# Performance work log

Measured on AMD Instinct MI355X. Metric: run time of the kernel, lower is better.

## Reference

```python
import jax, jax.numpy as jnp
import numpy as np
from jax import lax


def setup_inputs() -> dict:
    key = jax.random.key(0)
    k1, k2, k3 = jax.random.split(key, 3)
    B, Ci, Co, K, H, W = 8, 512, 512, 3, 32, 32
    x = jax.random.normal(k1, (B, Ci, H, W), dtype=jnp.float32)
    y_s = jax.random.normal(k2, (B, Ci), dtype=jnp.float32)
    weight = jax.random.normal(k3, (Co, Ci, K, K), dtype=jnp.float32)  # scale_init = 1 (equal_lr)
    bias = jnp.zeros((Co,), dtype=jnp.float32)
    return {"x": x, "y_s": y_s, "weight": weight, "bias": bias}


def reference(x, y_s, weight, bias):
    # equal_lr=True -> runtime scale = (in_channels * k^2) ** -0.5
    Co, Ci, K, _ = weight.shape
    scale_forward = (Ci * K * K) ** -0.5
    w = scale_forward * weight  # [Co, Ci, K, K]

    # Fused StyleGAN2 trick (mathematically identical to per-sample grouped conv):
    # conv(x, y_s[b,i]*w[o,i]) == conv(x * y_s, w); demod divides by per-(b,o) norm.
    x_mod = x * y_s[:, :, None, None]
    out = lax.conv_general_dilated(
        x_mod, w,
        window_strides=(1, 1),
        padding=((1, 1), (1, 1)),
        rhs_dilation=(1, 1),
        dimension_numbers=("NCHW", "OIHW", "NCHW"),
    )  # [B, Co, H, W]

    # demod=True: x_s[b,o] = sqrt(sum_{i,kh,kw} (y_s[b,i]*w[o,i,kh,kw])^2 + 1e-8)
    w2 = jnp.sum(w * w, axis=(2, 3))  # [Co, Ci]
    xs = jnp.sqrt(jnp.einsum("bi,oi->bo", y_s * y_s, w2) + 1e-8)  # [B, Co]
    out = out / xs[:, :, None, None] + bias[None, :, None, None]
    return out
```

## Files before the change

kernel.cpp:

```cpp
#include <hip/hip_runtime.h>

typedef __attribute__((ext_vector_type(8))) short short8;
typedef __attribute__((ext_vector_type(4))) float f32x4;

#define RCP_OFF   0
#define WPRE_OFF  16384
#define XM_OFF    4734976

__device__ __forceinline__ unsigned short f2bf(float f) {
  unsigned int u = __float_as_uint(f);
  u += 0x7FFFu + ((u >> 16) & 1u);
  return (unsigned short)(u >> 16);
}

__device__ __forceinline__ void gload_lds16(const void* g, void* l) {
  __builtin_amdgcn_global_load_lds(
      (__attribute__((address_space(1))) void*)g,
      (__attribute__((address_space(3))) void*)l, 16, 0, 0);
}

__global__ __launch_bounds__(256) void prep_kernel(
    const float* __restrict__ x, const float* __restrict__ ys,
    const float* __restrict__ w,
    unsigned short* __restrict__ xm, unsigned short* __restrict__ wpre,
    float* __restrict__ rcp) {
  int bid = blockIdx.x;
  int tid = threadIdx.x;

  if (bid < 512) {
    int half = bid & 1;
    int h = (bid >> 1) & 31;
    int b = bid >> 6;
    __shared__ float tile[256][33];
    int ci0 = half * 256;
#pragma unroll
    for (int r = 0; r < 32; ++r) {
      int ci = r * 8 + (tid >> 5);
      int wcol = tid & 31;
      float v = x[(((size_t)b * 512 + ci0 + ci) * 32 + h) * 32 + wcol];
      tile[ci][wcol] = v * ys[b * 512 + ci0 + ci];
    }
    __syncthreads();
    int g0 = half * 32;
    for (int r = 0; r < 5; ++r) {
      int idx = r * 256 + tid;
      if (idx < 1088) {
        int gl = idx / 34;
        int col = idx - gl * 34;
        short8 v = {0,0,0,0,0,0,0,0};
        if (col != 0 && col != 33) {
          int wcol = col - 1;
#pragma unroll
          for (int j = 0; j < 8; ++j)
            v[j] = (short)f2bf(tile[gl * 8 + j][wcol]);
        }
        size_t off = ((((size_t)b * 64 + g0 + gl) * 34 + (h + 1)) * 34 + col) * 8;
        *reinterpret_cast<short8*>(xm + off) = v;
      }
    }
    if (h == 0 || h == 31) {
      int hp = (h == 0) ? 0 : 33;
      for (int r = 0; r < 5; ++r) {
        int idx = r * 256 + tid;
        if (idx < 1088) {
          int gl = idx / 34;
          int col = idx - gl * 34;
          short8 z = {0,0,0,0,0,0,0,0};
          size_t off = ((((size_t)b * 64 + g0 + gl) * 34 + hp) * 34 + col) * 8;
          *reinterpret_cast<short8*>(xm + off) = z;
        }
      }
    }
  } else if (bid < 640) {
    int pid = bid - 512;
    int coh = pid & 1;
    int kb = (pid >> 1) & 7;
    int c = pid >> 4;
    int co = coh * 256 + tid;
    int ci0 = c * 64 + kb * 8;
    const float* wp = w + (size_t)co * 4608 + (size_t)ci0 * 9;
    float v[72];
    const f32x4* wp4 = reinterpret_cast<const f32x4*>(wp);
#pragma unroll
    for (int i = 0; i < 18; ++i) {
      f32x4 q = wp4[i];
      v[i * 4 + 0] = q[0]; v[i * 4 + 1] = q[1]; v[i * 4 + 2] = q[2]; v[i * 4 + 3] = q[3];
    }
    const float scale = 1.4731391274719738e-02f;
#pragma unroll
    for (int t = 0; t < 9; ++t) {
      short8 s;
#pragma unroll
      for (int j = 0; j < 8; ++j) s[j] = (short)f2bf(scale * v[j * 9 + t]);
      *reinterpret_cast<short8*>(wpre + ((((size_t)c * 9 + t) * 8 + kb) * 512 + co) * 8) = s;
    }
  } else {
    int pid = bid - 640;
    int wv = tid >> 6;
    int lane = tid & 63;
    int o = pid * 4 + wv;
    const float* wp = w + (size_t)o * 4608 + (size_t)lane * 72;
    const float scale2 = 1.0f / 4608.0f;
    float w2[8];
#pragma unroll
    for (int j = 0; j < 8; ++j) {
      float s = 0.f;
#pragma unroll
      for (int k = 0; k < 9; ++k) { float vv = wp[j * 9 + k]; s += vv * vv; }
      w2[j] = s * scale2;
    }
#pragma unroll
    for (int b = 0; b < 8; ++b) {
      float p = 0.f;
#pragma unroll
      for (int j = 0; j < 8; ++j) {
        float y = ys[b * 512 + lane * 8 + j];
        p += y * y * w2[j];
      }
#pragma unroll
      for (int off = 32; off > 0; off >>= 1) p += __shfl_down(p, off);
      if (lane == 0) rcp[b * 512 + o] = 1.0f / sqrtf(p + 1e-8f);
    }
  }
}

__global__ __launch_bounds__(512, 1) void conv_main(
    const unsigned short* __restrict__ wpre,
    const unsigned short* __restrict__ xm,
    const float* __restrict__ rcp,
    const float* __restrict__ bias,
    float* __restrict__ out)
{
  __shared__ __align__(16) char smem[52224];

  int bid = blockIdx.x;
  int xcd = bid & 7;
  int j0 = bid >> 3;
  int cog = xcd >> 1;
  int sp = (xcd & 1) * 32 + j0;
  int b = sp >> 3;
  int hg = sp & 7;
  int tid = threadIdx.x;
  int lane = tid & 63;
  int wv = tid >> 6;
  int wc = wv & 1;
  int wr = (wv >> 1) & 1;
  int kp = wv >> 2;
  int l15 = lane & 15, l4 = lane >> 4;

  f32x4 acc[4][4];
#pragma unroll
  for (int i = 0; i < 4; ++i)
#pragma unroll
    for (int jj = 0; jj < 4; ++jj) { f32x4 z = {0.f,0.f,0.f,0.f}; acc[i][jj] = z; }

  const unsigned short* xmb = xm + (size_t)b * (64 * 34 * 34 * 8);
  const unsigned short* wbase =
      wpre + ((size_t)(kp * 4 + l4) * 512 + cog * 128 + wr * 64 + l15) * 8;
  const int bbase = (kp * 4 + l4) * 3264 + wc * 2 * 544 + l15 * 16;

  auto stageX = [&](int c, int buf) {
    char* xb = smem + buf * 26112;
#pragma unroll
    for (int r = 0; r < 4; ++r) {
      int idx = r * 512 + tid;
      if (idx < 1632) {
        int kb = idx / 204;
        int rem = idx - kb * 204;
        int rr = rem / 34;
        int col = rem - rr * 34;
        const unsigned short* src =
            xmb + (((size_t)(c * 8 + kb) * 34 + hg * 4 + rr) * 34 + col) * 8;
        gload_lds16(src, xb + idx * 16);
      }
    }
  };

  auto loadA = [&](int ct, short8 (&a)[4]) {
    const unsigned short* p = wbase + (size_t)ct * 32768;
#pragma unroll
    for (int mi = 0; mi < 4; ++mi)
      a[mi] = *reinterpret_cast<const short8*>(p + mi * 128);
  };

  auto loadB = [&](const char* xb, int t, short8 (&f)[4]) {
    int kh = t / 3, kw = t % 3;
#pragma unroll
    for (int nj = 0; nj < 4; ++nj) {
      int imm = ((nj >> 1) + kh) * 544 + (nj & 1) * 256 + kw * 16;
      f[nj] = *reinterpret_cast<const short8*>(xb + bbase + imm);
    }
  };

  short8 X[4], Y[4], Z[4];

  stageX(0, 0);
  loadA(0, X);
  loadA(1, Y);
  __syncthreads();

  for (int cc = 0; cc < 8; ++cc) {
    const int c = cc;
    const char* xb = smem + (c & 1) * 26112;
    if (c < 7) stageX(c + 1, (c + 1) & 1);
    short8 Bp[4], Bq[4];
    loadB(xb, 0, Bp);
#pragma unroll
    for (int t = 0; t < 9; ++t) {
      int ct = c * 9 + t;
      short8 (&curA)[4] = (t % 3 == 0) ? X : ((t % 3 == 1) ? Y : Z);
      short8 (&nxtA)[4] = (t % 3 == 0) ? Z : ((t % 3 == 1) ? X : Y);
      short8 (&curB)[4] = (t & 1) ? Bq : Bp;
      short8 (&nxtB)[4] = (t & 1) ? Bp : Bq;
      if (ct < 70) loadA(ct + 2, nxtA);
      if (t < 8) loadB(xb, t + 1, nxtB);
#pragma unroll
      for (int nj = 0; nj < 4; ++nj)
#pragma unroll
        for (int mi = 0; mi < 4; ++mi)
          acc[mi][nj] = __builtin_amdgcn_mfma_f32_16x16x32_bf16(curA[mi], curB[nj], acc[mi][nj], 0, 0, 0);
    }
    if (c < 7) {
      asm volatile("s_waitcnt vmcnt(8) lgkmcnt(0)" ::: "memory");
      __builtin_amdgcn_s_barrier();
      asm volatile("" ::: "memory");
    }
  }
  __syncthreads();

#pragma unroll
  for (int p = 0; p < 2; ++p) {
    if (kp == 1 && wr == p) {
#pragma unroll
      for (int mi = 0; mi < 4; ++mi)
#pragma unroll
        for (int nj = 0; nj < 4; ++nj)
          *reinterpret_cast<f32x4*>(smem + wc * 16384 + (mi * 4 + nj) * 1024 + lane * 16) = acc[mi][nj];
    }
    __syncthreads();
    if (kp == 0 && wr == p) {
#pragma unroll
      for (int mi = 0; mi < 4; ++mi)
#pragma unroll
        for (int nj = 0; nj < 4; ++nj) {
          f32x4 v = *reinterpret_cast<const f32x4*>(smem + wc * 16384 + (mi * 4 + nj) * 1024 + lane * 16);
          acc[mi][nj] = acc[mi][nj] + v;
        }
    }
    __syncthreads();
  }

  if (kp == 0) {
    const float* rcpb = rcp + b * 512;
#pragma unroll
    for (int mi = 0; mi < 4; ++mi) {
      int ob = cog * 128 + wr * 64 + mi * 16 + l4 * 4;
      float rc[4], bi[4];
#pragma unroll
      for (int jj = 0; jj < 4; ++jj) { rc[jj] = rcpb[ob + jj]; bi[jj] = bias[ob + jj]; }
#pragma unroll
      for (int nj = 0; nj < 4; ++nj) {
        int row4 = wc * 2 + (nj >> 1);
        int wcol = (nj & 1) * 16 + l15;
        int h = hg * 4 + row4;
#pragma unroll
        for (int jj = 0; jj < 4; ++jj)
          out[(((size_t)b * 512 + ob + jj) * 32 + h) * 32 + wcol] = acc[mi][nj][jj] * rc[jj] + bi[jj];
      }
    }
  }
}

extern "C" void kernel_launch(void* const* d_in, const int* in_sizes, int n_in,
                              void* d_out, int out_size, void* d_ws, size_t ws_size,
                              hipStream_t stream) {
  const float* x    = (const float*)d_in[0];
  const float* ys   = (const float*)d_in[1];
  const float* w    = (const float*)d_in[2];
  const float* bias = (const float*)d_in[3];
  float* out = (float*)d_out;
  char* ws = (char*)d_ws;
  float* rcp = (float*)(ws + RCP_OFF);
  unsigned short* wpre = (unsigned short*)(ws + WPRE_OFF);
  unsigned short* xm   = (unsigned short*)(ws + XM_OFF);

  prep_kernel<<<768, 256, 0, stream>>>(x, ys, w, xm, wpre, rcp);
  conv_main<<<256, 512, 0, stream>>>(wpre, xm, rcp, bias, out);
}
```

Measured before the change: 58.59 us.

## Split conv reduction across two blocks with atomic accumulation into zeroed output

The input-channel reduction is split in half across two blocks (split-K), doubling the conv grid from 256 to 512 blocks so more CUs are occupied. Each block reduces its partials in LDS as before, then atomically adds its scaled result into the output, with only one half adding the bias. The prep kernel gains extra blocks that zero the output first. This trades extra atomic traffic and an output-zeroing pass for better occupancy, and the launch bound is relaxed to allow more blocks per CU.

```diff
diff --git a/kernel.cpp b/kernel.cpp
--- a/kernel.cpp
+++ b/kernel.cpp
@@ -23,7 +23,7 @@
     const float* __restrict__ x, const float* __restrict__ ys,
     const float* __restrict__ w,
     unsigned short* __restrict__ xm, unsigned short* __restrict__ wpre,
-    float* __restrict__ rcp) {
+    float* __restrict__ rcp, float* __restrict__ out) {
   int bid = blockIdx.x;
   int tid = threadIdx.x;
 
@@ -94,7 +94,7 @@
       for (int j = 0; j < 8; ++j) s[j] = (short)f2bf(scale * v[j * 9 + t]);
       *reinterpret_cast<short8*>(wpre + ((((size_t)c * 9 + t) * 8 + kb) * 512 + co) * 8) = s;
     }
-  } else {
+  } else if (bid < 768) {
     int pid = bid - 640;
     int wv = tid >> 6;
     int lane = tid & 63;
@@ -121,10 +121,18 @@
       for (int off = 32; off > 0; off >>= 1) p += __shfl_down(p, off);
       if (lane == 0) rcp[b * 512 + o] = 1.0f / sqrtf(p + 1e-8f);
     }
+  } else {
+    int pid = bid - 768;
+    f32x4* o4 = reinterpret_cast<f32x4*>(out);
+    f32x4 z = {0.f, 0.f, 0.f, 0.f};
+    int base = pid * 256 + tid;
+#pragma unroll
+    for (int i = 0; i < 16; ++i)
+      o4[(size_t)i * 65536 + base] = z;
   }
 }
 
-__global__ __launch_bounds__(512, 1) void conv_main(
+__global__ __launch_bounds__(512, 4) void conv_main(
     const unsigned short* __restrict__ wpre,
     const unsigned short* __restrict__ xm,
     const float* __restrict__ rcp,
@@ -134,10 +142,9 @@
   __shared__ __align__(16) char smem[52224];
 
   int bid = blockIdx.x;
-  int xcd = bid & 7;
-  int j0 = bid >> 3;
-  int cog = xcd >> 1;
-  int sp = (xcd & 1) * 32 + j0;
+  int kp = bid & 1;
+  int cog = (bid >> 1) & 3;
+  int sp = bid >> 3;
   int b = sp >> 3;
   int hg = sp & 7;
   int tid = threadIdx.x;
@@ -145,7 +152,7 @@
   int wv = tid >> 6;
   int wc = wv & 1;
   int wr = (wv >> 1) & 1;
-  int kp = wv >> 2;
+  int kq = wv >> 2;
   int l15 = lane & 15, l4 = lane >> 4;
 
   f32x4 acc[4][4];
@@ -156,10 +163,10 @@
 
   const unsigned short* xmb = xm + (size_t)b * (64 * 34 * 34 * 8);
   const unsigned short* wbase =
-      wpre + ((size_t)(kp * 4 + l4) * 512 + cog * 128 + wr * 64 + l15) * 8;
-  const int bbase = (kp * 4 + l4) * 3264 + wc * 2 * 544 + l15 * 16;
-
-  auto stageX = [&](int c, int buf) {
+      wpre + ((size_t)(kq * 4 + l4) * 512 + cog * 128 + wr * 64 + l15) * 8;
+  const int bbase = (kq * 4 + l4) * 3264 + wc * 2 * 544 + l15 * 16;
+
+  auto stageX = [&](int cg, int buf) {
     char* xb = smem + buf * 26112;
 #pragma unroll
     for (int r = 0; r < 4; ++r) {
@@ -170,14 +177,14 @@
         int rr = rem / 34;
         int col = rem - rr * 34;
         const unsigned short* src =
-            xmb + (((size_t)(c * 8 + kb) * 34 + hg * 4 + rr) * 34 + col) * 8;
+            xmb + (((size_t)(cg * 8 + kb) * 34 + hg * 4 + rr) * 34 + col) * 8;
         gload_lds16(src, xb + idx * 16);
       }
     }
   };
 
-  auto loadA = [&](int ct, short8 (&a)[4]) {
-    const unsigned short* p = wbase + (size_t)ct * 32768;
+  auto loadA = [&](int ctg, short8 (&a)[4]) {
+    const unsigned short* p = wbase + (size_t)ctg * 32768;
 #pragma unroll
     for (int mi = 0; mi < 4; ++mi)
       a[mi] = *reinterpret_cast<const short8*>(p + mi * 128);
@@ -193,26 +200,28 @@
   };
 
   short8 X[4], Y[4], Z[4];
-
-  stageX(0, 0);
-  loadA(0, X);
-  loadA(1, Y);
-  __syncthreads();
-
-  for (int cc = 0; cc < 8; ++cc) {
-    const int c = cc;
+  const int tap0 = kp * 36;
+
+  stageX(kp * 4, 0);
+  loadA(tap0, X);
+  loadA(tap0 + 1, Y);
+  asm volatile("s_waitcnt vmcnt(8)" ::: "memory");
+  __builtin_amdgcn_s_barrier();
+  asm volatile("" ::: "memory");
+
+  for (int c = 0; c < 4; ++c) {
     const char* xb = smem + (c & 1) * 26112;
-    if (c < 7) stageX(c + 1, (c + 1) & 1);
+    if (c < 3) stageX(kp * 4 + c + 1, (c + 1) & 1);
     short8 Bp[4], Bq[4];
     loadB(xb, 0, Bp);
 #pragma unroll
     for (int t = 0; t < 9; ++t) {
-      int ct = c * 9 + t;
+      int lt = c * 9 + t;
       short8 (&curA)[4] = (t % 3 == 0) ? X : ((t % 3 == 1) ? Y : Z);
       short8 (&nxtA)[4] = (t % 3 == 0) ? Z : ((t % 3 == 1) ? X : Y);
       short8 (&curB)[4] = (t & 1) ? Bq : Bp;
       short8 (&nxtB)[4] = (t & 1) ? Bp : Bq;
-      if (ct < 70) loadA(ct + 2, nxtA);
+      if (lt < 34) loadA(tap0 + lt + 2, nxtA);
       if (t < 8) loadB(xb, t + 1, nxtB);
 #pragma unroll
       for (int nj = 0; nj < 4; ++nj)
@@ -220,7 +229,7 @@
         for (int mi = 0; mi < 4; ++mi)
           acc[mi][nj] = __builtin_amdgcn_mfma_f32_16x16x32_bf16(curA[mi], curB[nj], acc[mi][nj], 0, 0, 0);
     }
-    if (c < 7) {
+    if (c < 3) {
       asm volatile("s_waitcnt vmcnt(8) lgkmcnt(0)" ::: "memory");
       __builtin_amdgcn_s_barrier();
       asm volatile("" ::: "memory");
@@ -230,7 +239,7 @@
 
 #pragma unroll
   for (int p = 0; p < 2; ++p) {
-    if (kp == 1 && wr == p) {
+    if (kq == 1 && wr == p) {
 #pragma unroll
       for (int mi = 0; mi < 4; ++mi)
 #pragma unroll
@@ -238,7 +247,7 @@
           *reinterpret_cast<f32x4*>(smem + wc * 16384 + (mi * 4 + nj) * 1024 + lane * 16) = acc[mi][nj];
     }
     __syncthreads();
-    if (kp == 0 && wr == p) {
+    if (kq == 0 && wr == p) {
 #pragma unroll
       for (int mi = 0; mi < 4; ++mi)
 #pragma unroll
@@ -250,14 +259,17 @@
     __syncthreads();
   }
 
-  if (kp == 0) {
+  if (kq == 0) {
     const float* rcpb = rcp + b * 512;
 #pragma unroll
     for (int mi = 0; mi < 4; ++mi) {
       int ob = cog * 128 + wr * 64 + mi * 16 + l4 * 4;
       float rc[4], bi[4];
 #pragma unroll
-      for (int jj = 0; jj < 4; ++jj) { rc[jj] = rcpb[ob + jj]; bi[jj] = bias[ob + jj]; }
+      for (int jj = 0; jj < 4; ++jj) {
+        rc[jj] = rcpb[ob + jj];
+        bi[jj] = kp ? 0.f : bias[ob + jj];
+      }
 #pragma unroll
       for (int nj = 0; nj < 4; ++nj) {
         int row4 = wc * 2 + (nj >> 1);
@@ -265,7 +277,8 @@
         int h = hg * 4 + row4;
 #pragma unroll
         for (int jj = 0; jj < 4; ++jj)
-          out[(((size_t)b * 512 + ob + jj) * 32 + h) * 32 + wcol] = acc[mi][nj][jj] * rc[jj] + bi[jj];
+          atomicAdd(&out[(((size_t)b * 512 + ob + jj) * 32 + h) * 32 + wcol],
+                    acc[mi][nj][jj] * rc[jj] + bi[jj]);
       }
     }
   }
@@ -284,6 +297,6 @@
   unsigned short* wpre = (unsigned short*)(ws + WPRE_OFF);
   unsigned short* xm   = (unsigned short*)(ws + XM_OFF);
 
-  prep_kernel<<<768, 256, 0, stream>>>(x, ys, w, xm, wpre, rcp);
-  conv_main<<<256, 512, 0, stream>>>(wpre, xm, rcp, bias, out);
-}
+  prep_kernel<<<1024, 256, 0, stream>>>(x, ys, w, xm, wpre, rcp, out);
+  conv_main<<<512, 512, 0, stream>>>(wpre, xm, rcp, bias, out);
+}
```

Result: slower. 84.46 us (+44.2%).
